# Kernel optimization log

Hardware: AMD Instinct MI355X
Metric: run time of the kernel (lower is better)

## Reference

```python
import jax, jax.numpy as jnp
import numpy as np

N_TOKENS = 65536
D_MODEL = 1024
N_EXP = 64
TOP_K = 8
ROUTER_TEMP = 1.0  # select_temp=None -> selection uses router_temp
GUMBEL_TAU = 1.0   # unused: inference=True skips gumbel noise
EPS_T = 1e-06
EPS_D = 1e-09


def setup_inputs() -> dict:
    key = jax.random.key(0)
    k_h, k_w = jax.random.split(key)
    h = jax.random.normal(k_h, (N_TOKENS, D_MODEL), dtype=jnp.float32)
    # eqx.nn.Linear weight layout: [out_features, in_features] = [n_exp, d_model]
    W = jax.random.normal(k_w, (N_EXP, D_MODEL), dtype=jnp.float32) / np.sqrt(D_MODEL)
    token_mask = jnp.ones((N_TOKENS,), dtype=bool)
    return {"h": h, "W": W, "token_mask": token_mask}


def reference(h, W, token_mask):
    # inference=True path: no dropout, no gumbel noise.
    logits_clean = jnp.einsum("nd,ed->ne", h, W)  # [N, n_exp]

    # selection logits (select_temp defaults to router_temp)
    t_sel = jnp.clip(ROUTER_TEMP, EPS_T, None)
    logits_sel = logits_clean / t_sel
    logits_sel = jnp.where(token_mask[:, None], logits_sel, -jnp.inf)

    # top-k mask over experts
    _, idx = jax.lax.top_k(logits_sel, TOP_K)  # [N, k]
    n = logits_clean.shape[0]
    mask_full = jnp.zeros((n, N_EXP), dtype=bool).at[
        jnp.arange(n)[:, None], idx
    ].set(True)
    mask_full = mask_full & token_mask[:, None]

    # mixing probs: softmax(logits/T), zero masked tokens, renormalize over top-k
    t_mix = jnp.clip(ROUTER_TEMP, EPS_T, None)
    dense = jax.nn.softmax(logits_clean / t_mix, axis=-1)
    dense = jnp.where(token_mask[:, None], dense, 0.0)
    masked = jnp.where(mask_full, dense, 0.0)
    denom = jnp.clip(masked.sum(axis=-1, keepdims=True), EPS_D, None)
    probs = masked / denom
    probs = jnp.where(token_mask[:, None], probs, 0.0)

    return mask_full, probs, logits_clean, logits_sel
```

## Files before the change

kernel.cpp:

```cpp
#include <hip/hip_runtime.h>
#include <cmath>

#define NTOK 65536
#define DMOD 1024
#define NEXP 64
#define TOPK 8
#define BTOK 128
#define KCH  64
#define NCH  (DMOD / KCH)
#define HSTR 96

__device__ __forceinline__ bool tok_mask(const void* tm, int t, int mmode) {
    return mmode == 0 ? (((const unsigned char*)tm)[t] != 0)
                      : (((const unsigned int*)tm)[t] != 0u);
}

__global__ __launch_bounds__(128, 1)
void router_v9(const float* __restrict__ h,
               const float* __restrict__ W,
               const void* __restrict__ tmask,
               float* __restrict__ out)
{
    __shared__ float smem[BTOK * HSTR + 64 * HSTR];
    __shared__ float sm_m0[BTOK], sm_inv[BTOK];
    __shared__ unsigned long long mb[BTOK];

    float* h_s = smem;
    float* w_s = smem + BTOK * HSTR;
    float (*ls)[65] = reinterpret_cast<float(*)[65]>(smem);

    const int tid  = threadIdx.x;
    const int lane = tid & 63;
    const int wave = tid >> 6;
    const int tg   = tid & 15;
    const int eg   = tid >> 4;
    const int t0   = blockIdx.x * BTOK;

    const unsigned int mw = *(const unsigned int*)tmask;
    const int mmode = (mw == 0x01010101u) ? 0 : 1;

    float acc[8][8];
#pragma unroll
    for (int i = 0; i < 8; ++i)
#pragma unroll
        for (int j = 0; j < 8; ++j) acc[i][j] = 0.f;

    const int hb = tg * 8 * HSTR + 4 * (tg & 7);
    const int wb = eg * 8 * HSTR + 4 * (eg & 7);

    for (int c = 0; c < NCH; ++c) {
        const int kc = c * KCH;

#pragma unroll
        for (int p = 0; p < 16; ++p) {
            const int g   = p * 128 + tid;
            const int row = g >> 4;
            const int c4  = (g & 15) * 4;
            const float4 v = *reinterpret_cast<const float4*>(
                h + (size_t)(t0 + row) * DMOD + kc + c4);
            *reinterpret_cast<float4*>(&h_s[row * HSTR + 4 * ((row >> 3) & 7) + c4]) = v;
        }
#pragma unroll
        for (int p = 0; p < 8; ++p) {
            const int g   = p * 128 + tid;
            const int row = g >> 4;
            const int c4  = (g & 15) * 4;
            const float4 v = *reinterpret_cast<const float4*>(
                W + ((size_t)row << 10) + kc + c4);
            *reinterpret_cast<float4*>(&w_s[row * HSTR + 4 * ((row >> 3) & 7) + c4]) = v;
        }
        __syncthreads();

#pragma unroll 4
        for (int k4 = 0; k4 < KCH / 4; ++k4) {
            float4 hv[8], wv[8];
#pragma unroll
            for (int i = 0; i < 8; ++i)
                hv[i] = *reinterpret_cast<const float4*>(&h_s[hb + i * HSTR + k4 * 4]);
#pragma unroll
            for (int j = 0; j < 8; ++j)
                wv[j] = *reinterpret_cast<const float4*>(&w_s[wb + j * HSTR + k4 * 4]);
#pragma unroll
            for (int i = 0; i < 8; ++i) {
#pragma unroll
                for (int j = 0; j < 8; ++j) {
                    float a = acc[i][j];
                    a = fmaf(hv[i].x, wv[j].x, a);
                    a = fmaf(hv[i].y, wv[j].y, a);
                    a = fmaf(hv[i].z, wv[j].z, a);
                    a = fmaf(hv[i].w, wv[j].w, a);
                    acc[i][j] = a;
                }
            }
        }
        __syncthreads();
    }

#pragma unroll
    for (int i = 0; i < 8; ++i)
#pragma unroll
        for (int j = 0; j < 8; ++j)
            ls[tg * 8 + i][eg * 8 + j] = acc[i][j];

    __syncthreads();

    const size_t P = (size_t)NTOK * NEXP;
    float* __restrict__ o_mask = out;
    float* __restrict__ o_prob = out + P;
    float* __restrict__ o_lc   = out + 2 * P;
    float* __restrict__ o_lsl  = out + 3 * P;
    const size_t base = (size_t)t0 * NEXP;

#pragma unroll 8
    for (int i = 0; i < 64; ++i) {
        const int f = i * 128 + tid;
        const int t = f >> 6, e = f & 63;
        const float lv = ls[t][e];
        const bool tmt = tok_mask(tmask, t0 + t, mmode);
        o_lc[base + f]  = lv;
        o_lsl[base + f] = tmt ? lv : -INFINITY;
    }

    {
        const int lt = wave * 64 + lane;
        const bool tm = tok_mask(tmask, t0 + lt, mmode);

        unsigned long long bits = 0ULL;
        float m0 = -INFINITY;
        for (int r = 0; r < TOPK; ++r) {
            float bv = -INFINITY; int bi = 0;
            for (int e = 0; e < 64; ++e) {
                if ((bits >> e) & 1ULL) continue;
                const float x = ls[lt][e];
                if (x > bv) { bv = x; bi = e; }
            }
            bits |= 1ULL << bi;
            if (r == 0) m0 = bv;
        }

        float ssum = 0.f;
        for (int e = 0; e < 64; ++e)
            if ((bits >> e) & 1ULL) ssum += expf(ls[lt][e] - m0);

        sm_m0[lt]  = m0;
        sm_inv[lt] = 1.0f / ssum;
        mb[lt] = tm ? bits : 0ULL;
    }

    __syncthreads();

#pragma unroll 8
    for (int i = 0; i < 64; ++i) {
        const int f = i * 128 + tid;
        const int t = f >> 6, e = f & 63;
        const unsigned long long bt = mb[t];
        const bool sel = ((bt >> e) & 1ULL) != 0ULL;
        o_prob[base + f] = sel ? expf(ls[t][e] - sm_m0[t]) * sm_inv[t] : 0.f;
        o_mask[base + f] = sel ? 1.0f : 0.0f;
    }
}

extern "C" void kernel_launch(void* const* d_in, const int* in_sizes, int n_in,
                              void* d_out, int out_size, void* d_ws, size_t ws_size,
                              hipStream_t stream)
{
    const float* h = (const float*)d_in[0];
    const float* W = (const float*)d_in[1];
    const void*  tmask = (const void*)d_in[2];
    float* out = (float*)d_out;

    hipLaunchKernelGGL(router_v9, dim3(NTOK / BTOK), dim3(128), 0, stream,
                       h, W, tmask, out);
}
```

Measured before the change: 229.7 us.

## Shrink token tile, raise occupancy, and vectorize output stores

Halves the token tile to 64 and doubles threads per block to 256, so each thread holds a 2x8 accumulator instead of 8x8. This allows several blocks per CU and hides global-memory latency for the memory-bound h stream. Global loads are staged through registers before the shared stores, and the output writes use float4. The trade-offs are that W is reloaded for every 64 tokens, shared memory now uses padded stride-65 rows, and top-k runs on only one wave while the other idles.

```diff
diff --git a/kernel.cpp b/kernel.cpp
--- a/kernel.cpp
+++ b/kernel.cpp
@@ -5,83 +5,75 @@
 #define DMOD 1024
 #define NEXP 64
 #define TOPK 8
-#define BTOK 128
+#define BTOK 64
 #define KCH  64
 #define NCH  (DMOD / KCH)
-#define HSTR 96
+#define STR  65
 
 __device__ __forceinline__ bool tok_mask(const void* tm, int t, int mmode) {
     return mmode == 0 ? (((const unsigned char*)tm)[t] != 0)
                       : (((const unsigned int*)tm)[t] != 0u);
 }
 
-__global__ __launch_bounds__(128, 1)
-void router_v9(const float* __restrict__ h,
-               const float* __restrict__ W,
-               const void* __restrict__ tmask,
-               float* __restrict__ out)
+__global__ __launch_bounds__(256, 4)
+void router_v10(const float* __restrict__ h,
+                const float* __restrict__ W,
+                const void* __restrict__ tmask,
+                float* __restrict__ out)
 {
-    __shared__ float smem[BTOK * HSTR + 64 * HSTR];
+    __shared__ float h_s[BTOK][STR];
+    __shared__ float w_s[NEXP][STR];
     __shared__ float sm_m0[BTOK], sm_inv[BTOK];
     __shared__ unsigned long long mb[BTOK];
-
-    float* h_s = smem;
-    float* w_s = smem + BTOK * HSTR;
-    float (*ls)[65] = reinterpret_cast<float(*)[65]>(smem);
 
     const int tid  = threadIdx.x;
     const int lane = tid & 63;
     const int wave = tid >> 6;
-    const int tg   = tid & 15;
-    const int eg   = tid >> 4;
+    const int tg   = tid >> 3;
+    const int eg   = tid & 7;
     const int t0   = blockIdx.x * BTOK;
 
     const unsigned int mw = *(const unsigned int*)tmask;
     const int mmode = (mw == 0x01010101u) ? 0 : 1;
 
-    float acc[8][8];
+    float acc[2][8];
 #pragma unroll
-    for (int i = 0; i < 8; ++i)
+    for (int i = 0; i < 2; ++i)
 #pragma unroll
         for (int j = 0; j < 8; ++j) acc[i][j] = 0.f;
 
-    const int hb = tg * 8 * HSTR + 4 * (tg & 7);
-    const int wb = eg * 8 * HSTR + 4 * (eg & 7);
+    const int sro = tid >> 4;
+    const int sc  = (tid & 15) * 4;
 
     for (int c = 0; c < NCH; ++c) {
         const int kc = c * KCH;
 
+        float4 ht[4], wt[4];
 #pragma unroll
-        for (int p = 0; p < 16; ++p) {
-            const int g   = p * 128 + tid;
-            const int row = g >> 4;
-            const int c4  = (g & 15) * 4;
-            const float4 v = *reinterpret_cast<const float4*>(
-                h + (size_t)(t0 + row) * DMOD + kc + c4);
-            *reinterpret_cast<float4*>(&h_s[row * HSTR + 4 * ((row >> 3) & 7) + c4]) = v;
+        for (int p = 0; p < 4; ++p) {
+            const int row = p * 16 + sro;
+            ht[p] = *reinterpret_cast<const float4*>(h + (size_t)(t0 + row) * DMOD + kc + sc);
+            wt[p] = *reinterpret_cast<const float4*>(W + ((size_t)row << 10) + kc + sc);
         }
 #pragma unroll
-        for (int p = 0; p < 8; ++p) {
-            const int g   = p * 128 + tid;
-            const int row = g >> 4;
-            const int c4  = (g & 15) * 4;
-            const float4 v = *reinterpret_cast<const float4*>(
-                W + ((size_t)row << 10) + kc + c4);
-            *reinterpret_cast<float4*>(&w_s[row * HSTR + 4 * ((row >> 3) & 7) + c4]) = v;
+        for (int p = 0; p < 4; ++p) {
+            const int row = p * 16 + sro;
+            *reinterpret_cast<float4*>(&h_s[row][sc]) = ht[p];
+            *reinterpret_cast<float4*>(&w_s[row][sc]) = wt[p];
         }
         __syncthreads();
 
 #pragma unroll 4
         for (int k4 = 0; k4 < KCH / 4; ++k4) {
-            float4 hv[8], wv[8];
+            float4 hv[2], wv[8];
 #pragma unroll
-            for (int i = 0; i < 8; ++i)
-                hv[i] = *reinterpret_cast<const float4*>(&h_s[hb + i * HSTR + k4 * 4]);
+            for (int i = 0; i < 2; ++i)
+                hv[i] = *reinterpret_cast<const float4*>(&h_s[tg * 2 + i][k4 * 4]);
 #pragma unroll
             for (int j = 0; j < 8; ++j)
-                wv[j] = *reinterpret_cast<const float4*>(&w_s[wb + j * HSTR + k4 * 4]);
+                wv[j] = *reinterpret_cast<const float4*>(&w_s[eg * 8 + j][k4 * 4]);
 #pragma unroll
-            for (int i = 0; i < 8; ++i) {
+            for (int i = 0; i < 2; ++i) {
 #pragma unroll
                 for (int j = 0; j < 8; ++j) {
                     float a = acc[i][j];
@@ -96,11 +88,12 @@
         __syncthreads();
     }
 
+    float (*ls)[STR] = h_s;
 #pragma unroll
-    for (int i = 0; i < 8; ++i)
+    for (int i = 0; i < 2; ++i)
 #pragma unroll
         for (int j = 0; j < 8; ++j)
-            ls[tg * 8 + i][eg * 8 + j] = acc[i][j];
+            ls[tg * 2 + i][eg * 8 + j] = acc[i][j];
 
     __syncthreads();
 
@@ -111,18 +104,24 @@
     float* __restrict__ o_lsl  = out + 3 * P;
     const size_t base = (size_t)t0 * NEXP;
 
-#pragma unroll 8
-    for (int i = 0; i < 64; ++i) {
-        const int f = i * 128 + tid;
-        const int t = f >> 6, e = f & 63;
-        const float lv = ls[t][e];
+#pragma unroll
+    for (int p = 0; p < 4; ++p) {
+        const int g  = p * 256 + tid;
+        const int t  = g >> 4;
+        const int e4 = (g & 15) * 4;
+        const float4 lv = *reinterpret_cast<const float4*>(&ls[t][e4]);
         const bool tmt = tok_mask(tmask, t0 + t, mmode);
-        o_lc[base + f]  = lv;
-        o_lsl[base + f] = tmt ? lv : -INFINITY;
+        float4 sv;
+        sv.x = tmt ? lv.x : -INFINITY;
+        sv.y = tmt ? lv.y : -INFINITY;
+        sv.z = tmt ? lv.z : -INFINITY;
+        sv.w = tmt ? lv.w : -INFINITY;
+        *reinterpret_cast<float4*>(&o_lc[base + (size_t)g * 4])  = lv;
+        *reinterpret_cast<float4*>(&o_lsl[base + (size_t)g * 4]) = sv;
     }
 
-    {
-        const int lt = wave * 64 + lane;
+    if (wave == 0) {
+        const int lt = lane;
         const bool tm = tok_mask(tmask, t0 + lt, mmode);
 
         unsigned long long bits = 0ULL;
@@ -149,14 +148,29 @@
 
     __syncthreads();
 
-#pragma unroll 8
-    for (int i = 0; i < 64; ++i) {
-        const int f = i * 128 + tid;
-        const int t = f >> 6, e = f & 63;
+#pragma unroll
+    for (int p = 0; p < 4; ++p) {
+        const int g  = p * 256 + tid;
+        const int t  = g >> 4;
+        const int e4 = (g & 15) * 4;
+        const float4 lv = *reinterpret_cast<const float4*>(&ls[t][e4]);
         const unsigned long long bt = mb[t];
-        const bool sel = ((bt >> e) & 1ULL) != 0ULL;
-        o_prob[base + f] = sel ? expf(ls[t][e] - sm_m0[t]) * sm_inv[t] : 0.f;
-        o_mask[base + f] = sel ? 1.0f : 0.0f;
+        const float m0 = sm_m0[t], inv = sm_inv[t];
+        float4 pv, mv;
+        const bool s0 = (bt >> (e4 + 0)) & 1ULL;
+        const bool s1 = (bt >> (e4 + 1)) & 1ULL;
+        const bool s2 = (bt >> (e4 + 2)) & 1ULL;
+        const bool s3 = (bt >> (e4 + 3)) & 1ULL;
+        pv.x = s0 ? expf(lv.x - m0) * inv : 0.f;
+        pv.y = s1 ? expf(lv.y - m0) * inv : 0.f;
+        pv.z = s2 ? expf(lv.z - m0) * inv : 0.f;
+        pv.w = s3 ? expf(lv.w - m0) * inv : 0.f;
+        mv.x = s0 ? 1.f : 0.f;
+        mv.y = s1 ? 1.f : 0.f;
+        mv.z = s2 ? 1.f : 0.f;
+        mv.w = s3 ? 1.f : 0.f;
+        *reinterpret_cast<float4*>(&o_prob[base + (size_t)g * 4]) = pv;
+        *reinterpret_cast<float4*>(&o_mask[base + (size_t)g * 4]) = mv;
     }
 }
 
@@ -169,6 +183,6 @@
     const void*  tmask = (const void*)d_in[2];
     float* out = (float*)d_out;
 
-    hipLaunchKernelGGL(router_v9, dim3(NTOK / BTOK), dim3(128), 0, stream,
+    hipLaunchKernelGGL(router_v10, dim3(NTOK / BTOK), dim3(256), 0, stream,
                        h, W, tmask, out);
 }
```

Measured after the change: 283.7 us. +23.5%, slower.
